# Kernel optimization log

Hardware: AMD Instinct MI355X
Metric: run time of the kernel (lower is better)

The kernel has to match this reference:

```python
import jax, jax.numpy as jnp
import numpy as np


def setup_inputs() -> dict:
    key = jax.random.key(0)
    B, N = 32, 262144
    z = jax.random.uniform(key, (B, N, 3), dtype=jnp.float32)
    return {"z": z}


def reference(z):
    # order == 'xyz': lexicographic sort of the N points by (x, y, z),
    # x most significant. jnp.lexsort treats the LAST key as primary,
    # so pass (z_key, y_key, x_key). Sorts along axis=-1 (points),
    # batched over B for free.
    keys = (z[:, :, 2], z[:, :, 1], z[:, :, 0])  # each [B, N]
    idx_pa = jnp.lexsort(keys, axis=-1)          # [B, N] permutation: sorted -> original
    # Original computes torch.sort(gather(arange, idx_pa))[1], which is the
    # inverse permutation of idx_pa; argsort of a permutation inverts it.
    idx_re = jnp.argsort(idx_pa, axis=-1)        # [B, N] original -> sorted position
    return idx_pa, idx_re
```

## Files before the change

### kernel.cpp

```cpp
#include <hip/hip_runtime.h>
#include <stdint.h>

typedef unsigned int u32;
typedef unsigned long long u64;
typedef unsigned char u8;

#define BROWS 32
#define NPTS  262144
#define LOG_NPTS 18
#define CB 256
#define RCAP 1280
#define ROWSTRIDE_FIX (CB * RCAP)
#define CCAP 1536
#define FB2 1024

#define MCH 8192
#define MWG 1024
#define TCH 8192
#define TWG 1024

__device__ __forceinline__ u32 g18_of(float z0) {
    int b = (int)(z0 * 262144.0f);
    return (u32)(b < 0 ? 0 : (b > 262143 ? 262143 : b));
}

__global__ __launch_bounds__(256) void hist_kernel(const float* __restrict__ z,
                                                   u32* __restrict__ counts) {
    __shared__ u32 h[CB];
    for (int i = threadIdx.x; i < CB; i += 256) h[i] = 0;
    __syncthreads();
    int r = blockIdx.x >> 6;
    int c = blockIdx.x & 63;
    size_t base = ((size_t)r << LOG_NPTS) + (size_t)c * 4096;
    for (int k = 0; k < 16; ++k) {
        float z0 = z[(base + (size_t)(k * 256 + threadIdx.x)) * 3];
        atomicAdd(&h[g18_of(z0) >> 10], 1u);
    }
    __syncthreads();
    for (int i = threadIdx.x; i < CB; i += 256)
        if (h[i]) atomicAdd(&counts[r * CB + i], h[i]);
}

__global__ __launch_bounds__(256) void scan_dense(const u32* __restrict__ counts,
                                                  u32* __restrict__ offsets,
                                                  u32* __restrict__ gcur) {
    int r = blockIdx.x, t = threadIdx.x;
    __shared__ u32 sc[CB];
    u32 v = counts[r * CB + t];
    sc[t] = v;
    __syncthreads();
    u32 own = v;
    for (int off = 1; off < CB; off <<= 1) {
        u32 a = (t >= off) ? sc[t - off] : 0;
        __syncthreads();
        sc[t] += a;
        __syncthreads();
    }
    u32 ex = sc[t] - own;
    offsets[r * CB + t] = ex;
    gcur[r * CB + t] = ex;
}

__global__ void init_fixed(u32* __restrict__ gcur, u32* __restrict__ tcur) {
    int i = blockIdx.x * 256 + threadIdx.x;
    gcur[i] = (u32)(i & 255) * RCAP;
    tcur[i] = 0;
}

__global__ __launch_bounds__(256) void scan_fixed(const u32* __restrict__ gcur,
                                                  u32* __restrict__ offsets,
                                                  u32* __restrict__ counts) {
    int r = blockIdx.x, t = threadIdx.x;
    __shared__ u32 sc[CB];
    u32 cnt = gcur[r * CB + t] - (u32)t * RCAP;
    if (cnt > RCAP) cnt = RCAP;
    counts[r * CB + t] = cnt;
    sc[t] = cnt;
    __syncthreads();
    u32 own = cnt;
    for (int off = 1; off < CB; off <<= 1) {
        u32 a = (t >= off) ? sc[t - off] : 0;
        __syncthreads();
        sc[t] += a;
        __syncthreads();
    }
    offsets[r * CB + t] = sc[t] - own;
}

__global__ __launch_bounds__(MWG) void ms_scatter(const float* __restrict__ z,
                                                  u32* __restrict__ gcur,
                                                  u64* __restrict__ recK8,
                                                  u32* __restrict__ recI4,
                                                  int fixedMode) {
    __shared__ u32 h[CB], sc[CB], gb[CB], wtot[4];
    __shared__ u64 r8[MCH];
    int t = threadIdx.x;
    int r = blockIdx.x >> 5;
    int c = blockIdx.x & 31;
    if (t < CB) h[t] = 0;
    __syncthreads();

    u32 base_pt = (u32)(c * MCH + t * 8);
    const float4* zf4 = (const float4*)(z + ((size_t)r << LOG_NPTS) * 3 + (size_t)base_pt * 3);
    float4 f[6];
#pragma unroll
    for (int j = 0; j < 6; ++j) f[j] = zf4[j];
    const float* ff = (const float*)f;

    u64 mh[8];
    u32 mi[8], mpk[8];
#pragma unroll
    for (int k = 0; k < 8; ++k) {
        float f0 = ff[3 * k], f1 = ff[3 * k + 1];
        u32 k0 = __float_as_uint(f0), k1 = __float_as_uint(f1);
        mh[k] = ((u64)k0 << 32) | k1;
        mi[k] = base_pt + (u32)k;
        u32 b = g18_of(f0) >> 10;
        u32 arr = atomicAdd(&h[b], 1u);
        mpk[k] = (b << 16) | arr;
    }
    __syncthreads();
    u32 scan_s = 0, scan_v = 0;
    int lane = t & 63, wv = t >> 6;
    if (t < CB) {
        scan_v = h[t];
        scan_s = scan_v;
        for (int off = 1; off < 64; off <<= 1) {
            u32 o = __shfl_up(scan_s, off, 64);
            if (lane >= off) scan_s += o;
        }
        if (lane == 63) wtot[wv] = scan_s;
    }
    __syncthreads();
    if (t < CB) {
        u32 wb = 0;
        if (wv > 0) wb += wtot[0];
        if (wv > 1) wb += wtot[1];
        if (wv > 2) wb += wtot[2];
        sc[t] = wb + scan_s - scan_v;
        gb[t] = atomicAdd(&gcur[r * CB + t], h[t]);
    }
    __syncthreads();
    size_t rowrec = fixedMode ? (size_t)r * ROWSTRIDE_FIX : ((size_t)r << LOG_NPTS);

#pragma unroll
    for (int k = 0; k < 8; ++k) {
        u32 b = mpk[k] >> 16, arr = mpk[k] & 0xFFFFu;
        r8[sc[b] + arr] = mh[k];
    }
    __syncthreads();
#pragma unroll
    for (int k = 0; k < 8; ++k) {
        u32 s = (u32)(k * MWG + t);
        u64 v = r8[s];
        u32 b = g18_of(__uint_as_float((u32)(v >> 32))) >> 10;
        u32 local = s - sc[b];
        u32 dst = gb[b] + local;
        if (!fixedMode || dst < (b + 1u) * (u32)RCAP)
            recK8[rowrec + dst] = v;
    }
    __syncthreads();
    u32* ri = (u32*)r8;
#pragma unroll
    for (int k = 0; k < 8; ++k) {
        u32 b = mpk[k] >> 16, arr = mpk[k] & 0xFFFFu;
        ri[sc[b] + arr] = (b << 18) | mi[k];
    }
    __syncthreads();
#pragma unroll
    for (int k = 0; k < 8; ++k) {
        u32 s = (u32)(k * MWG + t);
        u32 v = ri[s];
        u32 b = v >> 18;
        u32 local = s - sc[b];
        u32 dst = gb[b] + local;
        if (!fixedMode || dst < (b + 1u) * (u32)RCAP)
            recI4[rowrec + dst] = v & 0x3FFFFu;
    }
}

__global__ __launch_bounds__(256) void fine_sort(const u64* __restrict__ recK8,
                                                 const u32* __restrict__ recI4,
                                                 const float* __restrict__ z,
                                                 const u32* __restrict__ offsets,
                                                 const u32* __restrict__ counts,
                                                 int* __restrict__ out_pa,
                                                 int fixedMode) {
    __shared__ u64 k8[CCAP];
    __shared__ u32 ki[CCAP];
    __shared__ u32 fh[FB2], fex[FB2], wtot[4];
    int t = threadIdx.x;
    int g = blockIdx.x;
    int r = g >> 8;
    int cbk = g & 255;
    size_t rowrec = fixedMode ? (size_t)r * ROWSTRIDE_FIX : ((size_t)r << LOG_NPTS);
    u32 rdstart = fixedMode ? (u32)cbk * RCAP : offsets[g];
    u32 wrstart = offsets[g];
    u32 count = counts[g];
    u32 cap = fixedMode ? (u32)RCAP : (u32)CCAP;
    if (count > cap) count = cap;
    for (int i = t; i < FB2; i += 256) fh[i] = 0;
    __syncthreads();

    u64 rh[6];
    u32 rid[6], rpk[6];
#pragma unroll
    for (int k = 0; k < 6; ++k) {
        u32 s = (u32)t + (u32)k * 256u;
        rpk[k] = 0xFFFFFFFFu;
        if (s < count) {
            u64 hi = recK8[rowrec + rdstart + s];
            u32 id = recI4[rowrec + rdstart + s];
            rh[k] = hi; rid[k] = id;
            u32 fb = g18_of(__uint_as_float((u32)(hi >> 32))) & (FB2 - 1);
            u32 arr = atomicAdd(&fh[fb], 1u);
            rpk[k] = (fb << 16) | arr;
        }
    }
    __syncthreads();
    {
        u32 v0 = fh[4 * t], v1 = fh[4 * t + 1], v2 = fh[4 * t + 2], v3 = fh[4 * t + 3];
        u32 tsum = v0 + v1 + v2 + v3;
        u32 s = tsum;
        int lane = t & 63, w = t >> 6;
        for (int off = 1; off < 64; off <<= 1) {
            u32 o = __shfl_up(s, off, 64);
            if (lane >= off) s += o;
        }
        if (lane == 63) wtot[w] = s;
        __syncthreads();
        u32 wbase = 0;
        if (w > 0) wbase += wtot[0];
        if (w > 1) wbase += wtot[1];
        if (w > 2) wbase += wtot[2];
        u32 ex = wbase + s - tsum;
        fex[4 * t] = ex;
        fex[4 * t + 1] = ex + v0;
        fex[4 * t + 2] = ex + v0 + v1;
        fex[4 * t + 3] = ex + v0 + v1 + v2;
    }
    __syncthreads();
#pragma unroll
    for (int k = 0; k < 6; ++k) {
        if (rpk[k] != 0xFFFFFFFFu) {
            u32 fb = rpk[k] >> 16, arr = rpk[k] & 0xFFFFu;
            u32 p = fex[fb] + arr;
            k8[p] = rh[k];
            ki[p] = rid[k];
        }
    }
    __syncthreads();

    size_t orow = (size_t)r << LOG_NPTS;
    size_t zrow = ((size_t)r << LOG_NPTS) * 3;
#pragma unroll
    for (int k = 0; k < 6; ++k) {
        if (rpk[k] == 0xFFFFFFFFu) continue;
        u32 fb = rpk[k] >> 16;
        u32 cnt = fh[fb];
        u32 rank = 0;
        if (cnt > 1) {
            u32 base = fex[fb];
            u64 e8 = rh[k];
            u32 ei = rid[k];
            for (u32 j = 0; j < cnt; ++j) {
                u64 b8 = k8[base + j];
                if (b8 < e8) { ++rank; continue; }
                if (b8 == e8) {
                    u32 bi = ki[base + j];
                    if (bi != ei) {
                        u32 bk2 = __float_as_uint(z[zrow + (size_t)bi * 3 + 2]);
                        u32 ek2 = __float_as_uint(z[zrow + (size_t)ei * 3 + 2]);
                        rank += (bk2 < ek2) || (bk2 == ek2 && bi < ei);
                    }
                }
            }
        }
        u32 pos = fex[fb] + rank;
        out_pa[orow + wrstart + pos] = (int)rid[k];
    }
}

__global__ __launch_bounds__(TWG) void trans_ms(const int* __restrict__ out_pa,
                                                u32* __restrict__ tcur,
                                                u32* __restrict__ pairs) {
    __shared__ u32 h[CB], sc[CB], gb[CB], wtot[4];
    __shared__ u32 reord[TCH];
    __shared__ u8 rb8[TCH];
    int t = threadIdx.x;
    int r = blockIdx.x >> 5;
    int c = blockIdx.x & 31;
    if (t < CB) h[t] = 0;
    __syncthreads();
    u32 mpk[8], mv[8];
#pragma unroll
    for (int k = 0; k < 8; ++k) {
        u32 p = (u32)(c * TCH + k * TWG + t);
        u32 si = (u32)out_pa[((size_t)r << LOG_NPTS) + p];
        u32 b = si >> 10;
        mv[k] = ((si & 1023u) << 18) | p;
        u32 arr = atomicAdd(&h[b], 1u);
        mpk[k] = (b << 16) | arr;
    }
    __syncthreads();
    u32 scan_s = 0, scan_v = 0;
    int lane = t & 63, wv = t >> 6;
    if (t < CB) {
        scan_v = h[t];
        scan_s = scan_v;
        for (int off = 1; off < 64; off <<= 1) {
            u32 o = __shfl_up(scan_s, off, 64);
            if (lane >= off) scan_s += o;
        }
        if (lane == 63) wtot[wv] = scan_s;
    }
    __syncthreads();
    if (t < CB) {
        u32 wbase = 0;
        if (wv > 0) wbase += wtot[0];
        if (wv > 1) wbase += wtot[1];
        if (wv > 2) wbase += wtot[2];
        sc[t] = wbase + scan_s - scan_v;
        gb[t] = atomicAdd(&tcur[r * CB + t], h[t]);
    }
    __syncthreads();
#pragma unroll
    for (int k = 0; k < 8; ++k) {
        u32 b = mpk[k] >> 16, arr = mpk[k] & 0xFFFFu;
        u32 p = sc[b] + arr;
        reord[p] = mv[k];
        rb8[p] = (u8)b;
    }
    __syncthreads();
#pragma unroll
    for (int k = 0; k < 8; ++k) {
        u32 s = (u32)(k * TWG + t);
        u32 v = reord[s];
        u32 b = rb8[s];
        u32 local = s - sc[b];
        pairs[((size_t)r << LOG_NPTS) + (size_t)b * 1024 + gb[b] + local] = v;
    }
}

__global__ __launch_bounds__(256) void trans_write(const u32* __restrict__ pairs,
                                                   int* __restrict__ out_re) {
    __shared__ u32 buf[1024];
    int g = blockIdx.x;
    int r = g >> 8, b = g & 255;
    size_t base = ((size_t)r << LOG_NPTS) + (size_t)b * 1024;
#pragma unroll
    for (int k = 0; k < 4; ++k) {
        u32 v = pairs[base + (size_t)(k * 256 + threadIdx.x)];
        buf[v >> 18] = v & 0x3FFFFu;
    }
    __syncthreads();
#pragma unroll
    for (int k = 0; k < 4; ++k) {
        int j = k * 256 + threadIdx.x;
        out_re[base + (size_t)j] = (int)buf[j];
    }
}

extern "C" void kernel_launch(void* const* d_in, const int* in_sizes, int n_in,
                              void* d_out, int out_size, void* d_ws, size_t ws_size,
                              hipStream_t stream) {
    const float* z = (const float*)d_in[0];
    int* out_pa = (int*)d_out;
    int* out_re = out_pa + (size_t)BROWS * NPTS;

    char* ws = (char*)d_ws;
    u32* counts  = (u32*)(ws);
    u32* offsets = (u32*)(ws + (64u << 10));
    u32* gcur    = (u32*)(ws + (128u << 10));
    u32* tcur    = (u32*)(ws + (192u << 10));
    u64* recK8   = (u64*)(ws + (1u << 20));
    u32* recI4   = (u32*)(ws + (1u << 20) + (80ull << 20));
    u32* pairs   = (u32*)recK8;

    size_t need = (1ull << 20) + (121ull << 20);
    int fixedMode = (ws_size >= need) ? 1 : 0;

    if (fixedMode) {
        init_fixed<<<BROWS, 256, 0, stream>>>(gcur, tcur);
        ms_scatter<<<BROWS * 32, MWG, 0, stream>>>(z, gcur, recK8, recI4, 1);
        scan_fixed<<<BROWS, 256, 0, stream>>>(gcur, offsets, counts);
        fine_sort<<<BROWS * CB, 256, 0, stream>>>(recK8, recI4, z, offsets, counts, out_pa, 1);
    } else {
        hipMemsetAsync(counts, 0, (size_t)BROWS * CB * sizeof(u32), stream);
        hipMemsetAsync(tcur, 0, (size_t)BROWS * CB * sizeof(u32), stream);
        hist_kernel<<<BROWS * 64, 256, 0, stream>>>(z, counts);
        scan_dense<<<BROWS, 256, 0, stream>>>(counts, offsets, gcur);
        ms_scatter<<<BROWS * 32, MWG, 0, stream>>>(z, gcur, recK8, recI4, 0);
        fine_sort<<<BROWS * CB, 256, 0, stream>>>(recK8, recI4, z, offsets, counts, out_pa, 0);
    }
    trans_ms<<<BROWS * 32, TWG, 0, stream>>>(out_pa, tcur, pairs);
    trans_write<<<BROWS * CB, 256, 0, stream>>>(pairs, out_re);
}
```

Measured before the change: 141.1 us.

## Pack fine bucket and index into one 4-byte record, refetch keys from input

```diff
diff --git a/kernel.cpp b/kernel.cpp
--- a/kernel.cpp
+++ b/kernel.cpp
@@ -89,11 +89,11 @@
 
 __global__ __launch_bounds__(MWG) void ms_scatter(const float* __restrict__ z,
                                                   u32* __restrict__ gcur,
-                                                  u64* __restrict__ recK8,
-                                                  u32* __restrict__ recI4,
+                                                  u32* __restrict__ rec,
                                                   int fixedMode) {
     __shared__ u32 h[CB], sc[CB], gb[CB], wtot[4];
-    __shared__ u64 r8[MCH];
+    __shared__ u32 reord[MCH];
+    __shared__ u8 rb8[MCH];
     int t = threadIdx.x;
     int r = blockIdx.x >> 5;
     int c = blockIdx.x & 31;
@@ -107,15 +107,12 @@
     for (int j = 0; j < 6; ++j) f[j] = zf4[j];
     const float* ff = (const float*)f;
 
-    u64 mh[8];
-    u32 mi[8], mpk[8];
-#pragma unroll
-    for (int k = 0; k < 8; ++k) {
-        float f0 = ff[3 * k], f1 = ff[3 * k + 1];
-        u32 k0 = __float_as_uint(f0), k1 = __float_as_uint(f1);
-        mh[k] = ((u64)k0 << 32) | k1;
-        mi[k] = base_pt + (u32)k;
-        u32 b = g18_of(f0) >> 10;
+    u32 mpk[8], mv[8];
+#pragma unroll
+    for (int k = 0; k < 8; ++k) {
+        u32 g = g18_of(ff[3 * k]);
+        u32 b = g >> 10;
+        mv[k] = ((g & 1023u) << 18) | (base_pt + (u32)k);
         u32 arr = atomicAdd(&h[b], 1u);
         mpk[k] = (b << 16) | arr;
     }
@@ -141,53 +138,35 @@
         gb[t] = atomicAdd(&gcur[r * CB + t], h[t]);
     }
     __syncthreads();
+#pragma unroll
+    for (int k = 0; k < 8; ++k) {
+        u32 b = mpk[k] >> 16, arr = mpk[k] & 0xFFFFu;
+        u32 p = sc[b] + arr;
+        reord[p] = mv[k];
+        rb8[p] = (u8)b;
+    }
+    __syncthreads();
     size_t rowrec = fixedMode ? (size_t)r * ROWSTRIDE_FIX : ((size_t)r << LOG_NPTS);
-
-#pragma unroll
-    for (int k = 0; k < 8; ++k) {
-        u32 b = mpk[k] >> 16, arr = mpk[k] & 0xFFFFu;
-        r8[sc[b] + arr] = mh[k];
-    }
-    __syncthreads();
 #pragma unroll
     for (int k = 0; k < 8; ++k) {
         u32 s = (u32)(k * MWG + t);
-        u64 v = r8[s];
-        u32 b = g18_of(__uint_as_float((u32)(v >> 32))) >> 10;
+        u32 v = reord[s];
+        u32 b = rb8[s];
         u32 local = s - sc[b];
         u32 dst = gb[b] + local;
         if (!fixedMode || dst < (b + 1u) * (u32)RCAP)
-            recK8[rowrec + dst] = v;
-    }
-    __syncthreads();
-    u32* ri = (u32*)r8;
-#pragma unroll
-    for (int k = 0; k < 8; ++k) {
-        u32 b = mpk[k] >> 16, arr = mpk[k] & 0xFFFFu;
-        ri[sc[b] + arr] = (b << 18) | mi[k];
-    }
-    __syncthreads();
-#pragma unroll
-    for (int k = 0; k < 8; ++k) {
-        u32 s = (u32)(k * MWG + t);
-        u32 v = ri[s];
-        u32 b = v >> 18;
-        u32 local = s - sc[b];
-        u32 dst = gb[b] + local;
-        if (!fixedMode || dst < (b + 1u) * (u32)RCAP)
-            recI4[rowrec + dst] = v & 0x3FFFFu;
-    }
-}
-
-__global__ __launch_bounds__(256) void fine_sort(const u64* __restrict__ recK8,
-                                                 const u32* __restrict__ recI4,
+            rec[rowrec + dst] = v;
+    }
+}
+
+__global__ __launch_bounds__(256) void fine_sort(const u32* __restrict__ rec,
                                                  const float* __restrict__ z,
                                                  const u32* __restrict__ offsets,
                                                  const u32* __restrict__ counts,
                                                  int* __restrict__ out_pa,
                                                  int fixedMode) {
-    __shared__ u64 k8[CCAP];
     __shared__ u32 ki[CCAP];
+    __shared__ u32 zk0[CCAP], zk1[CCAP], zk2[CCAP];
     __shared__ u32 fh[FB2], fex[FB2], wtot[4];
     int t = threadIdx.x;
     int g = blockIdx.x;
@@ -202,17 +181,15 @@
     for (int i = t; i < FB2; i += 256) fh[i] = 0;
     __syncthreads();
 
-    u64 rh[6];
     u32 rid[6], rpk[6];
 #pragma unroll
     for (int k = 0; k < 6; ++k) {
         u32 s = (u32)t + (u32)k * 256u;
         rpk[k] = 0xFFFFFFFFu;
         if (s < count) {
-            u64 hi = recK8[rowrec + rdstart + s];
-            u32 id = recI4[rowrec + rdstart + s];
-            rh[k] = hi; rid[k] = id;
-            u32 fb = g18_of(__uint_as_float((u32)(hi >> 32))) & (FB2 - 1);
+            u32 v = rec[rowrec + rdstart + s];
+            u32 fb = v >> 18;
+            rid[k] = v & 0x3FFFFu;
             u32 arr = atomicAdd(&fh[fb], 1u);
             rpk[k] = (fb << 16) | arr;
         }
@@ -240,43 +217,47 @@
         fex[4 * t + 3] = ex + v0 + v1 + v2;
     }
     __syncthreads();
+
+    size_t zrow = ((size_t)r << LOG_NPTS) * 3;
+    u32 e0[6], e1[6], e2[6];
 #pragma unroll
     for (int k = 0; k < 6; ++k) {
-        if (rpk[k] != 0xFFFFFFFFu) {
-            u32 fb = rpk[k] >> 16, arr = rpk[k] & 0xFFFFu;
-            u32 p = fex[fb] + arr;
-            k8[p] = rh[k];
-            ki[p] = rid[k];
+        if (rpk[k] == 0xFFFFFFFFu) continue;
+        u32 fb = rpk[k] >> 16, arr = rpk[k] & 0xFFFFu;
+        u32 p = fex[fb] + arr;
+        ki[p] = rid[k];
+        if (fh[fb] > 1) {
+            size_t a = zrow + (size_t)rid[k] * 3;
+            u32 a0 = __float_as_uint(z[a]);
+            u32 a1 = __float_as_uint(z[a + 1]);
+            u32 a2 = __float_as_uint(z[a + 2]);
+            e0[k] = a0; e1[k] = a1; e2[k] = a2;
+            zk0[p] = a0; zk1[p] = a1; zk2[p] = a2;
         }
     }
     __syncthreads();
 
     size_t orow = (size_t)r << LOG_NPTS;
-    size_t zrow = ((size_t)r << LOG_NPTS) * 3;
 #pragma unroll
     for (int k = 0; k < 6; ++k) {
         if (rpk[k] == 0xFFFFFFFFu) continue;
         u32 fb = rpk[k] >> 16;
         u32 cnt = fh[fb];
-        u32 rank = 0;
+        u32 base = fex[fb];
+        u32 pos = base;
         if (cnt > 1) {
-            u32 base = fex[fb];
-            u64 e8 = rh[k];
-            u32 ei = rid[k];
+            u32 rank = 0;
+            u32 a0 = e0[k], a1 = e1[k], a2 = e2[k], ai = rid[k];
             for (u32 j = 0; j < cnt; ++j) {
-                u64 b8 = k8[base + j];
-                if (b8 < e8) { ++rank; continue; }
-                if (b8 == e8) {
-                    u32 bi = ki[base + j];
-                    if (bi != ei) {
-                        u32 bk2 = __float_as_uint(z[zrow + (size_t)bi * 3 + 2]);
-                        u32 ek2 = __float_as_uint(z[zrow + (size_t)ei * 3 + 2]);
-                        rank += (bk2 < ek2) || (bk2 == ek2 && bi < ei);
-                    }
-                }
+                u32 b0 = zk0[base + j], b1 = zk1[base + j], b2 = zk2[base + j];
+                u32 bi = ki[base + j];
+                bool less = (b0 < a0) ||
+                            (b0 == a0 && (b1 < a1 ||
+                             (b1 == a1 && (b2 < a2 || (b2 == a2 && bi < ai)))));
+                rank += less;
             }
-        }
-        u32 pos = fex[fb] + rank;
+            pos = base + rank;
+        }
         out_pa[orow + wrstart + pos] = (int)rid[k];
     }
 }
@@ -373,25 +354,24 @@
     u32* offsets = (u32*)(ws + (64u << 10));
     u32* gcur    = (u32*)(ws + (128u << 10));
     u32* tcur    = (u32*)(ws + (192u << 10));
-    u64* recK8   = (u64*)(ws + (1u << 20));
-    u32* recI4   = (u32*)(ws + (1u << 20) + (80ull << 20));
-    u32* pairs   = (u32*)recK8;
-
-    size_t need = (1ull << 20) + (121ull << 20);
+    u32* rec     = (u32*)(ws + (1u << 20));
+    u32* pairs   = (u32*)(ws + (1u << 20) + (48ull << 20));
+
+    size_t need = (1ull << 20) + (48ull << 20) + (32ull << 20);
     int fixedMode = (ws_size >= need) ? 1 : 0;
 
     if (fixedMode) {
         init_fixed<<<BROWS, 256, 0, stream>>>(gcur, tcur);
-        ms_scatter<<<BROWS * 32, MWG, 0, stream>>>(z, gcur, recK8, recI4, 1);
+        ms_scatter<<<BROWS * 32, MWG, 0, stream>>>(z, gcur, rec, 1);
         scan_fixed<<<BROWS, 256, 0, stream>>>(gcur, offsets, counts);
-        fine_sort<<<BROWS * CB, 256, 0, stream>>>(recK8, recI4, z, offsets, counts, out_pa, 1);
+        fine_sort<<<BROWS * CB, 256, 0, stream>>>(rec, z, offsets, counts, out_pa, 1);
     } else {
         hipMemsetAsync(counts, 0, (size_t)BROWS * CB * sizeof(u32), stream);
         hipMemsetAsync(tcur, 0, (size_t)BROWS * CB * sizeof(u32), stream);
         hist_kernel<<<BROWS * 64, 256, 0, stream>>>(z, counts);
         scan_dense<<<BROWS, 256, 0, stream>>>(counts, offsets, gcur);
-        ms_scatter<<<BROWS * 32, MWG, 0, stream>>>(z, gcur, recK8, recI4, 0);
-        fine_sort<<<BROWS * CB, 256, 0, stream>>>(recK8, recI4, z, offsets, counts, out_pa, 0);
+        ms_scatter<<<BROWS * 32, MWG, 0, stream>>>(z, gcur, rec, 0);
+        fine_sort<<<BROWS * CB, 256, 0, stream>>>(rec, z, offsets, counts, out_pa, 0);
     }
     trans_ms<<<BROWS * 32, TWG, 0, stream>>>(out_pa, tcur, pairs);
     trans_write<<<BROWS * CB, 256, 0, stream>>>(pairs, out_re);
```

Measured after the change: 165.8 us. +17.5%, slower.
